# Kernel tuning notes

Hardware: AMD Instinct MI355X
Metric: run time of the kernel (lower is better)

The kernel has to match this reference:

```python
import jax, jax.numpy as jnp
import numpy as np

N = 100000
E = 1600000
IN_C = 128
HID_C = 32
HEADS = 4
OUT_C = 64
NUM_CLASSES = 2
NUM_GRAPHS = 64
NEG_SLOPE = 0.2  # PyG GATConv default leaky_relu slope


def _segment_softmax(logits, seg, num_segments):
    # logits: [E, H], seg: [E] destination node ids
    m = jax.ops.segment_max(logits, seg, num_segments=num_segments)
    m = jnp.where(jnp.isfinite(m), m, 0.0)
    e = jnp.exp(logits - m[seg])
    s = jax.ops.segment_sum(e, seg, num_segments=num_segments)
    return e / (s[seg] + 1e-16)


def _gat_conv(x, src, dst, W, att_src, att_dst, bias, heads, ch, concat):
    n = x.shape[0]
    h = (x @ W).reshape(n, heads, ch)                 # [N, H, C]
    a_src = jnp.sum(h * att_src, axis=-1)             # [N, H]
    a_dst = jnp.sum(h * att_dst, axis=-1)             # [N, H]
    alpha = jax.nn.leaky_relu(a_src[src] + a_dst[dst], NEG_SLOPE)  # [E, H]
    alpha = _segment_softmax(alpha, dst, n)
    msg = h[src] * alpha[:, :, None]                  # [E, H, C]
    out = jax.ops.segment_sum(msg, dst, num_segments=n)  # [N, H, C]
    out = out.reshape(n, heads * ch) if concat else out.mean(axis=1)
    return out + bias


def setup_inputs() -> dict:
    key = jax.random.key(0)
    ks = jax.random.split(key, 12)
    x = jax.random.normal(ks[0], (N, IN_C), dtype=jnp.float32)
    edge_index = jax.random.randint(ks[1], (2, E), 0, N, dtype=jnp.int32)
    batch = jnp.sort(jax.random.randint(ks[2], (N,), 0, NUM_GRAPHS, dtype=jnp.int32))
    s1 = 1.0 / np.sqrt(IN_C)
    W1 = jax.random.uniform(ks[3], (IN_C, HEADS * HID_C), minval=-s1, maxval=s1, dtype=jnp.float32)
    att_src1 = jax.random.normal(ks[4], (HEADS, HID_C), dtype=jnp.float32) * 0.1
    att_dst1 = jax.random.normal(ks[5], (HEADS, HID_C), dtype=jnp.float32) * 0.1
    b1 = jnp.zeros((HEADS * HID_C,), dtype=jnp.float32)
    s2 = 1.0 / np.sqrt(HEADS * HID_C)
    W2 = jax.random.uniform(ks[6], (HEADS * HID_C, OUT_C), minval=-s2, maxval=s2, dtype=jnp.float32)
    att_src2 = jax.random.normal(ks[7], (1, OUT_C), dtype=jnp.float32) * 0.1
    att_dst2 = jax.random.normal(ks[8], (1, OUT_C), dtype=jnp.float32) * 0.1
    b2 = jnp.zeros((OUT_C,), dtype=jnp.float32)
    sc = 1.0 / np.sqrt(OUT_C)
    Wc = jax.random.uniform(ks[9], (OUT_C, NUM_CLASSES), minval=-sc, maxval=sc, dtype=jnp.float32)
    bc = jnp.zeros((NUM_CLASSES,), dtype=jnp.float32)
    return {"x": x, "edge_index": edge_index, "batch": batch,
            "W1": W1, "att_src1": att_src1, "att_dst1": att_dst1, "b1": b1,
            "W2": W2, "att_src2": att_src2, "att_dst2": att_dst2, "b2": b2,
            "Wc": Wc, "bc": bc}


def reference(x, edge_index, batch, W1, att_src1, att_dst1, b1,
              W2, att_src2, att_dst2, b2, Wc, bc):
    # PyG GATConv adds self-loops by default
    loops = jnp.arange(N, dtype=edge_index.dtype)
    src = jnp.concatenate([edge_index[0], loops])
    dst = jnp.concatenate([edge_index[1], loops])
    # eval mode: dropout is identity
    h = _gat_conv(x, src, dst, W1, att_src1, att_dst1, b1, HEADS, HID_C, True)
    h = jax.nn.elu(h)
    h = _gat_conv(h, src, dst, W2, att_src2, att_dst2, b2, 1, OUT_C, False)
    h = jax.nn.elu(h)
    # global mean pool over graphs
    sums = jax.ops.segment_sum(h, batch, num_segments=NUM_GRAPHS)
    cnts = jax.ops.segment_sum(jnp.ones((N, 1), h.dtype), batch, num_segments=NUM_GRAPHS)
    pooled = sums / jnp.maximum(cnts, 1.0)
    return pooled @ Wc + bc
```

## Files before the change

### kernel.cpp

```cpp
#include <hip/hip_runtime.h>
#include <math.h>


typedef __attribute__((ext_vector_type(8))) short bf16x8;
typedef __attribute__((ext_vector_type(4))) float f32x4;

__device__ __forceinline__ unsigned f2bf_rne(float x){
  unsigned u = __float_as_uint(x);
  return (u + 0x7fffu + ((u >> 16) & 1u)) >> 16;
}
__device__ __forceinline__ unsigned pk_bf2(float a, float b){
  return f2bf_rne(a) | (f2bf_rne(b) << 16);
}
__device__ __forceinline__ void unpack8(uint4 q, float* f){
  f[0] = __uint_as_float(q.x << 16);
  f[1] = __uint_as_float(q.x & 0xffff0000u);
  f[2] = __uint_as_float(q.y << 16);
  f[3] = __uint_as_float(q.y & 0xffff0000u);
  f[4] = __uint_as_float(q.z << 16);
  f[5] = __uint_as_float(q.z & 0xffff0000u);
  f[6] = __uint_as_float(q.w << 16);
  f[7] = __uint_as_float(q.w & 0xffff0000u);
}


#define CHUNKE 8192

__global__ __launch_bounds__(256) void k_bucketcount(
    const int* __restrict__ dst, int* __restrict__ bcnt, int e, int NB)
{
  __shared__ int hcnt[512];
  const int tid = threadIdx.x;
  for (int b = tid; b < 512; b += 256) hcnt[b] = 0;
  __syncthreads();
  const int lo = blockIdx.x * CHUNKE;
  const int hi = min(lo + CHUNKE, e);
  for (int i = lo + tid; i < hi; i += 256)
    atomicAdd(&hcnt[dst[i] >> 8], 1);
  __syncthreads();
  for (int b = tid; b < NB; b += 256)
    if (hcnt[b]) atomicAdd(&bcnt[b], hcnt[b]);
}

__global__ __launch_bounds__(512) void k_bucketscan(
    const int* __restrict__ bcnt, int* __restrict__ bbase,
    int* __restrict__ cur, int* __restrict__ off, int e, int n, int NB)
{
  __shared__ int sh[512];
  const int t = threadIdx.x;
  int v = (t < NB) ? bcnt[t] : 0;
  sh[t] = v;
  __syncthreads();
  for (int o = 1; o < 512; o <<= 1){
    int x = (t >= o) ? sh[t - o] : 0;
    __syncthreads();
    sh[t] += x;
    __syncthreads();
  }
  if (t < NB){
    int excl = sh[t] - v;
    bbase[t] = excl;
    cur[t]   = excl;
  }
  if (t == 0) off[n] = e;
}

__global__ __launch_bounds__(256) void k_partition(
    const int* __restrict__ src, const int* __restrict__ dst,
    int* __restrict__ cur, unsigned* __restrict__ packed, int e, int NB)
{
  __shared__ unsigned       recs[CHUNKE];
  __shared__ unsigned short bkt[CHUNKE];
  __shared__ int hcnt[512];
  __shared__ int hoff[512];
  __shared__ int hbase[512];

  const int tid = threadIdx.x;
  const int lo  = blockIdx.x * CHUNKE;
  const int hi  = min(lo + CHUNKE, e);
  const int cnt = hi - lo;

  hcnt[tid] = 0; hcnt[tid + 256] = 0;
  __syncthreads();
  for (int i = lo + tid; i < hi; i += 256)
    atomicAdd(&hcnt[dst[i] >> 8], 1);
  __syncthreads();

  hoff[tid] = hcnt[tid]; hoff[tid + 256] = hcnt[tid + 256];
  __syncthreads();
  for (int o = 1; o < 512; o <<= 1){
    int x0 = (tid >= o)       ? hoff[tid - o]       : 0;
    int x1 = (tid + 256 >= o) ? hoff[tid + 256 - o] : 0;
    __syncthreads();
    hoff[tid] += x0; hoff[tid + 256] += x1;
    __syncthreads();
  }

  int c0 = hcnt[tid], c1 = hcnt[tid + 256];
  int e0 = hoff[tid] - c0, e1 = hoff[tid + 256] - c1;
  hbase[tid]       = c0 ? atomicAdd(&cur[tid], c0)       : 0;
  hbase[tid + 256] = c1 ? atomicAdd(&cur[tid + 256], c1) : 0;
  __syncthreads();
  hoff[tid] = e0; hoff[tid + 256] = e1;
  hcnt[tid] = 0;  hcnt[tid + 256] = 0;
  __syncthreads();

  for (int i = lo + tid; i < hi; i += 256){
    int d = dst[i];
    int b = d >> 8;
    int p = hoff[b] + atomicAdd(&hcnt[b], 1);
    recs[p] = (unsigned)src[i] | ((unsigned)(d & 255) << 17);
    bkt[p]  = (unsigned short)b;
  }
  __syncthreads();

  for (int t = tid; t < cnt; t += 256){
    int b = bkt[t];
    packed[hbase[b] + t - hoff[b]] = recs[t];
  }
}

__global__ __launch_bounds__(256) void k_bucketbuild(
    const unsigned* __restrict__ packed, const int* __restrict__ bbase,
    const int* __restrict__ bcnt, int* __restrict__ off,
    int* __restrict__ csr, int n)
{
  __shared__ int lcnt[256];
  __shared__ int loff[256];
  const int b    = blockIdx.x;
  const int tid  = threadIdx.x;
  const int seg0 = bbase[b];
  const int scnt = bcnt[b];

  lcnt[tid] = 0;
  __syncthreads();
  for (int i = tid; i < scnt; i += 256)
    atomicAdd(&lcnt[packed[seg0 + i] >> 17], 1);
  __syncthreads();
  int v = lcnt[tid];
  loff[tid] = v;
  __syncthreads();
  for (int o = 1; o < 256; o <<= 1){
    int x = (tid >= o) ? loff[tid - o] : 0;
    __syncthreads();
    loff[tid] += x;
    __syncthreads();
  }
  int excl = loff[tid] - v;
  __syncthreads();
  loff[tid] = excl;
  lcnt[tid] = 0;
  int d = (b << 8) + tid;
  if (d < n) off[d] = seg0 + excl;
  __syncthreads();
  for (int i = tid; i < scnt; i += 256){
    unsigned rec = packed[seg0 + i];
    int doff = rec >> 17;
    int s    = rec & 0x1FFFF;
    int p    = atomicAdd(&lcnt[doff], 1);
    csr[seg0 + loff[doff] + p] = s;
  }
}


template<int OUTC, int HEADS, bool XBF16, typename XT>
__global__ __launch_bounds__(256) void k_gemm_mfma(
    const XT* __restrict__ X, const float* __restrict__ W,
    const float* __restrict__ att_s, const float* __restrict__ att_d,
    unsigned short* __restrict__ H, float* __restrict__ ASRC,
    float* __restrict__ ADST, int n)
{
  constexpr int K  = 128;
  constexpr int KC = 32;
  constexpr int CT = OUTC / 16;
  constexpr int RT = 16 / CT;
  constexpr int WROWS = RT * 16;
  constexpr int BROWS = WROWS * 4;

  __shared__ unsigned short Bs[OUTC][K + 8];
  __shared__ unsigned short As[BROWS][KC + 8];

  const int tid   = threadIdx.x;
  const int lane  = tid & 63;
  const int c15   = lane & 15;
  const int quad  = lane >> 4;
  const int warow = (tid >> 6) * WROWS;
  const int row0  = blockIdx.x * BROWS;

  f32x4 acc[CT][RT];
  #pragma unroll
  for (int ct = 0; ct < CT; ++ct)
    #pragma unroll
    for (int t = 0; t < RT; ++t)
      #pragma unroll
      for (int r = 0; r < 4; ++r) acc[ct][t][r] = 0.f;

  for (int idx = tid; idx < K * OUTC / 4; idx += 256){
    int k  = idx / (OUTC / 4);
    int c4 = (idx % (OUTC / 4)) * 4;
    float4 v = *(const float4*)&W[(size_t)k * OUTC + c4];
    Bs[c4 + 0][k] = (unsigned short)f2bf_rne(v.x);
    Bs[c4 + 1][k] = (unsigned short)f2bf_rne(v.y);
    Bs[c4 + 2][k] = (unsigned short)f2bf_rne(v.z);
    Bs[c4 + 3][k] = (unsigned short)f2bf_rne(v.w);
  }

  for (int kc = 0; kc < K; kc += KC){
    if (XBF16){
      for (int idx = tid; idx < BROWS * (KC / 8); idx += 256){
        int rr = idx / (KC / 8);
        int q  = idx % (KC / 8);
        int row = row0 + rr;
        uint4 v = make_uint4(0, 0, 0, 0);
        if (row < n) v = *(const uint4*)((const unsigned short*)X + (size_t)row * K + kc + q * 8);
        *(uint4*)&As[rr][q * 8] = v;
      }
    } else {
      for (int idx = tid; idx < BROWS * (KC / 4); idx += 256){
        int rr = idx / (KC / 4);
        int q  = idx % (KC / 4);
        int row = row0 + rr;
        float4 v = make_float4(0.f, 0.f, 0.f, 0.f);
        if (row < n) v = *(const float4*)((const float*)X + (size_t)row * K + kc + q * 4);
        *(uint2*)&As[rr][q * 4] = make_uint2(pk_bf2(v.x, v.y), pk_bf2(v.z, v.w));
      }
    }
    __syncthreads();

    bf16x8 af[RT];
    #pragma unroll
    for (int t = 0; t < RT; ++t)
      af[t] = *(const bf16x8*)&As[warow + t * 16 + c15][8 * quad];
    #pragma unroll
    for (int ct = 0; ct < CT; ++ct){
      bf16x8 bfr = *(const bf16x8*)&Bs[ct * 16 + c15][kc + 8 * quad];
      #pragma unroll
      for (int t = 0; t < RT; ++t)
        acc[ct][t] = __builtin_amdgcn_mfma_f32_16x16x32_bf16(af[t], bfr, acc[ct][t], 0, 0, 0);
    }
    __syncthreads();
  }

  float ats[CT], atd[CT];
  #pragma unroll
  for (int ct = 0; ct < CT; ++ct){
    ats[ct] = att_s[ct * 16 + c15];
    atd[ct] = att_d[ct * 16 + c15];
  }
  #pragma unroll
  for (int t = 0; t < RT; ++t){
    #pragma unroll
    for (int r = 0; r < 4; ++r){
      int row = row0 + warow + t * 16 + quad * 4 + r;
      float hs[HEADS], hd[HEADS];
      #pragma unroll
      for (int h = 0; h < HEADS; ++h){ hs[h] = 0.f; hd[h] = 0.f; }
      #pragma unroll
      for (int ct = 0; ct < CT; ++ct){
        float v = acc[ct][t][r];
        constexpr int CPH = OUTC / HEADS;
        int h = (ct * 16) / CPH;
        hs[h] = fmaf(v, ats[ct], hs[h]);
        hd[h] = fmaf(v, atd[ct], hd[h]);
      }
      #pragma unroll
      for (int h = 0; h < HEADS; ++h){
        #pragma unroll
        for (int s = 1; s < 16; s <<= 1){
          hs[h] += __shfl_xor(hs[h], s);
          hd[h] += __shfl_xor(hd[h], s);
        }
      }
      if (row < n){
        #pragma unroll
        for (int ct = 0; ct < CT; ++ct)
          H[(size_t)row * OUTC + ct * 16 + c15] = (unsigned short)f2bf_rne(acc[ct][t][r]);
        if (c15 == 0){
          #pragma unroll
          for (int h = 0; h < HEADS; ++h){
            ASRC[(size_t)row * HEADS + h] = hs[h];
            ADST[(size_t)row * HEADS + h] = hd[h];
          }
        }
      }
    }
  }
}


template<int CH, int HEADS, bool OUTBF16>
__global__ __launch_bounds__(256) void k_aggregate(
    const unsigned short* __restrict__ Hmsg, const float* __restrict__ ASRC,
    const float* __restrict__ ADST, const int* __restrict__ off,
    const int* __restrict__ csr, const float* __restrict__ bias,
    void* __restrict__ OUT, int n)
{
  constexpr int CL  = CH / 8;
  constexpr int DPB = 256 / CL;
  constexpr int CPH = CH / HEADS;
  constexpr int RQ  = CH / 8;

  const int tid = threadIdx.x;
  const int ld  = tid / CL;
  const int cl  = tid % CL;
  const int c0  = cl * 8;
  const int h   = c0 / CPH;
  const int d   = blockIdx.x * DPB + ld;
  if (d >= n) return;

  const uint4* Hv = (const uint4*)Hmsg;
  const float adst = ADST[d * HEADS + h];

  float acc[8];
  float wsum;
  {
    float t = ASRC[d * HEADS + h] + adst;
    float w = __expf(fmaxf(t, 0.2f * t));
    float f[8];
    unpack8(Hv[d * RQ + cl], f);
    #pragma unroll
    for (int j = 0; j < 8; ++j) acc[j] = w * f[j];
    wsum = w;
  }

  const int s0   = off[d];
  const int cnt  = off[d + 1] - s0;
  const int full = cnt & ~7;

  for (int p = 0; p < full; p += 8){
    int idx[8];
    #pragma unroll
    for (int j = 0; j < 8; ++j) idx[j] = csr[s0 + p + j];
    float av[8];
    #pragma unroll
    for (int j = 0; j < 8; ++j) av[j] = ASRC[idx[j] * HEADS + h];
    uint4 hq[8];
    #pragma unroll
    for (int j = 0; j < 8; ++j) hq[j] = Hv[idx[j] * RQ + cl];
    #pragma unroll
    for (int j = 0; j < 8; ++j){
      float t = av[j] + adst;
      float w = __expf(fmaxf(t, 0.2f * t));
      float f[8];
      unpack8(hq[j], f);
      #pragma unroll
      for (int q = 0; q < 8; ++q) acc[q] = fmaf(w, f[q], acc[q]);
      wsum += w;
    }
  }

  const int rem = cnt - full;
  if (rem){
    int  idx[8];
    bool ok[8];
    #pragma unroll
    for (int j = 0; j < 8; ++j){
      int q = csr[s0 + full + j];
      ok[j]  = j < rem;
      idx[j] = ok[j] ? q : 0;
    }
    float av[8];
    #pragma unroll
    for (int j = 0; j < 8; ++j) av[j] = ASRC[idx[j] * HEADS + h];
    uint4 hq[8];
    #pragma unroll
    for (int j = 0; j < 8; ++j) hq[j] = Hv[idx[j] * RQ + cl];
    #pragma unroll
    for (int j = 0; j < 8; ++j){
      float t = av[j] + adst;
      float w = __expf(fmaxf(t, 0.2f * t));
      w = ok[j] ? w : 0.f;
      float f[8];
      unpack8(hq[j], f);
      #pragma unroll
      for (int q = 0; q < 8; ++q) acc[q] = fmaf(w, f[q], acc[q]);
      wsum += w;
    }
  }

  const float inv = 1.f / (wsum + 1e-16f);
  float o[8];
  #pragma unroll
  for (int j = 0; j < 8; ++j){
    float v = acc[j] * inv + bias[c0 + j];
    o[j] = v > 0.f ? v : expm1f(v);
  }
  if (OUTBF16){
    uint4 q;
    q.x = pk_bf2(o[0], o[1]); q.y = pk_bf2(o[2], o[3]);
    q.z = pk_bf2(o[4], o[5]); q.w = pk_bf2(o[6], o[7]);
    *(uint4*)((unsigned short*)OUT + (size_t)d * CH + c0) = q;
  } else {
    float* Of = (float*)OUT;
    *(float4*)&Of[(size_t)d * CH + c0 + 0] = make_float4(o[0], o[1], o[2], o[3]);
    *(float4*)&Of[(size_t)d * CH + c0 + 4] = make_float4(o[4], o[5], o[6], o[7]);
  }
}


__global__ __launch_bounds__(256) void k_pool_partial(
    const float* __restrict__ H, const int* __restrict__ batch,
    float* __restrict__ sums, int n)
{
  constexpr int CHUNK = 256;
  const int c    = threadIdx.x & 63;
  const int slot = threadIdx.x >> 6;
  const int start = blockIdx.x * CHUNK;
  const int end   = min(start + CHUNK, n);

  float acc = 0.f;
  int cur = -1;
  for (int nn = start + slot; nn < end; nn += 4){
    int g = batch[nn];
    if (g != cur){
      if (cur >= 0) atomicAdd(&sums[cur * 64 + c], acc);
      acc = 0.f; cur = g;
    }
    acc += H[(size_t)nn * 64 + c];
  }
  if (cur >= 0) atomicAdd(&sums[cur * 64 + c], acc);
}

__global__ __launch_bounds__(128) void k_classify(
    const float* __restrict__ sums, const int* __restrict__ batch,
    const float* __restrict__ Wc, const float* __restrict__ bc,
    float* __restrict__ out, int n)
{
  int t = threadIdx.x;
  if (t >= 128) return;
  int g = t >> 1, cls = t & 1;
  int lo = 0, hi = n;
  while (lo < hi){ int m = (lo + hi) >> 1; if (batch[m] < g) lo = m + 1; else hi = m; }
  int s = lo;
  lo = s; hi = n;
  while (lo < hi){ int m = (lo + hi) >> 1; if (batch[m] < g + 1) lo = m + 1; else hi = m; }
  int cnt = lo - s;
  float inv = 1.f / (float)(cnt > 1 ? cnt : 1);
  float dot = 0.f;
  #pragma unroll
  for (int c = 0; c < 64; ++c) dot = fmaf(sums[g * 64 + c], Wc[c * 2 + cls], dot);
  out[g * 2 + cls] = dot * inv + bc[cls];
}


extern "C" void kernel_launch(void* const* d_in, const int* in_sizes, int n_in,
                              void* d_out, int out_size, void* d_ws, size_t ws_size,
                              hipStream_t stream)
{
  const float* x    = (const float*)d_in[0];
  const int*   edge = (const int*)  d_in[1];
  const int*   batch= (const int*)  d_in[2];
  const float* W1   = (const float*)d_in[3];
  const float* as1w = (const float*)d_in[4];
  const float* ad1w = (const float*)d_in[5];
  const float* b1   = (const float*)d_in[6];
  const float* W2   = (const float*)d_in[7];
  const float* as2w = (const float*)d_in[8];
  const float* ad2w = (const float*)d_in[9];
  const float* b2   = (const float*)d_in[10];
  const float* Wc   = (const float*)d_in[11];
  const float* bc   = (const float*)d_in[12];

  const int n = in_sizes[2];
  const int e = in_sizes[1] / 2;
  const int* esrc = edge;
  const int* edst = edge + e;
  const int NB = (n + 255) >> 8;

  unsigned short* h1  = (unsigned short*)d_ws;
  unsigned short* h1a = h1 + (size_t)n * 128;
  float* as1 = (float*)(h1a + (size_t)n * 128);
  float* ad1 = as1 + (size_t)n * 4;
  float* as2 = ad1 + (size_t)n * 4;
  float* ad2 = as2 + (size_t)n;
  float* sums = ad2 + (size_t)n;
  int*  bcnt  = (int*)(sums + 64 * 64);
  int*  cur   = bcnt + 512;
  int*  bbase = cur + 512;
  int*  off   = bbase + 512;
  unsigned* packed = (unsigned*)(off + n + 1);
  int*  csr   = (int*)(packed + e);

  const int eb = (e + CHUNKE - 1) / CHUNKE;

  hipMemsetAsync(sums, 0, (64 * 64 + 512) * 4, stream);
  k_bucketcount<<<eb, 256, 0, stream>>>(edst, bcnt, e, NB);
  k_bucketscan <<<1, 512, 0, stream>>>(bcnt, bbase, cur, off, e, n, NB);
  k_partition  <<<eb, 256, 0, stream>>>(esrc, edst, cur, packed, e, NB);
  k_bucketbuild<<<NB, 256, 0, stream>>>(packed, bbase, bcnt, off, csr, n);

  k_gemm_mfma<128, 4, false><<<(n + 127) / 128, 256, 0, stream>>>(
      x, W1, as1w, ad1w, h1, as1, ad1, n);
  k_aggregate<128, 4, true><<<(n + 15) / 16, 256, 0, stream>>>(
      h1, as1, ad1, off, csr, b1, (void*)h1a, n);

  unsigned short* h2 = h1;
  float* h2a = (float*)h1a;
  k_gemm_mfma<64, 1, true><<<(n + 255) / 256, 256, 0, stream>>>(
      h1a, W2, as2w, ad2w, h2, as2, ad2, n);
  k_aggregate<64, 1, false><<<(n + 31) / 32, 256, 0, stream>>>(
      h2, as2, ad2, off, csr, b2, (void*)h2a, n);

  k_pool_partial<<<(n + 255) / 256, 256, 0, stream>>>(h2a, batch, sums, n);
  k_classify<<<1, 128, 0, stream>>>(sums, batch, Wc, bc, (float*)d_out, n);
}
```

Measured before the change: 376.3 us.

## Fold attention vectors into GEMM as extra MFMA tile; multi-dst aggregate

Precomputes W·att_src and W·att_dst per head, stored as hi/lo bf16 split rows, inside an otherwise idle second block of the scan kernel. The GEMM then gets the attention logits from one extra 16-column MFMA tile instead of a per-row shuffle reduction over heads. The aggregate kernels also process four destination nodes per thread group with bias hoisted, cutting block count. This trades an extra MFMA tile and bf16-split precision for fewer shuffles, and adds serial per-thread work that may reduce latency hiding in the aggregation.

```diff
diff --git a/kernel.cpp b/kernel.cpp
--- a/kernel.cpp
+++ b/kernel.cpp
@@ -44,10 +44,56 @@
 
 __global__ __launch_bounds__(512) void k_bucketscan(
     const int* __restrict__ bcnt, int* __restrict__ bbase,
-    int* __restrict__ cur, int* __restrict__ off, int e, int n, int NB)
-{
+    int* __restrict__ cur, int* __restrict__ off, int e, int n, int NB,
+    const float* __restrict__ W1, const float* __restrict__ as1w,
+    const float* __restrict__ ad1w,
+    const float* __restrict__ W2, const float* __restrict__ as2w,
+    const float* __restrict__ ad2w,
+    unsigned short* __restrict__ wa1, unsigned short* __restrict__ wa2)
+{
+  const int t = threadIdx.x;
+
+  if (blockIdx.x == 1){
+    for (int i = t; i < 2048; i += 512) wa2[i] = 0;
+    __syncthreads();
+    {
+      int k = t >> 2, j = t & 3;
+      float ds = 0.f, dd = 0.f;
+      for (int cc = 0; cc < 32; ++cc){
+        float wv = W1[k * 128 + j * 32 + cc];
+        ds = fmaf(wv, as1w[j * 32 + cc], ds);
+        dd = fmaf(wv, ad1w[j * 32 + cc], dd);
+      }
+      unsigned hs_ = f2bf_rne(ds); float hsf = __uint_as_float(hs_ << 16);
+      unsigned ls_ = f2bf_rne(ds - hsf);
+      unsigned hd_ = f2bf_rne(dd); float hdf = __uint_as_float(hd_ << 16);
+      unsigned ld_ = f2bf_rne(dd - hdf);
+      wa1[(j     ) * 128 + k] = (unsigned short)hs_;
+      wa1[(j + 4 ) * 128 + k] = (unsigned short)ls_;
+      wa1[(j + 8 ) * 128 + k] = (unsigned short)hd_;
+      wa1[(j + 12) * 128 + k] = (unsigned short)ld_;
+    }
+    if (t < 128){
+      int k = t;
+      float ds = 0.f, dd = 0.f;
+      for (int cc = 0; cc < 64; ++cc){
+        float wv = W2[k * 64 + cc];
+        ds = fmaf(wv, as2w[cc], ds);
+        dd = fmaf(wv, ad2w[cc], dd);
+      }
+      unsigned hs_ = f2bf_rne(ds); float hsf = __uint_as_float(hs_ << 16);
+      unsigned ls_ = f2bf_rne(ds - hsf);
+      unsigned hd_ = f2bf_rne(dd); float hdf = __uint_as_float(hd_ << 16);
+      unsigned ld_ = f2bf_rne(dd - hdf);
+      wa2[ 0 * 128 + k] = (unsigned short)hs_;
+      wa2[ 4 * 128 + k] = (unsigned short)ls_;
+      wa2[ 8 * 128 + k] = (unsigned short)hd_;
+      wa2[12 * 128 + k] = (unsigned short)ld_;
+    }
+    return;
+  }
+
   __shared__ int sh[512];
-  const int t = threadIdx.x;
   int v = (t < NB) ? bcnt[t] : 0;
   sh[t] = v;
   __syncthreads();
@@ -166,18 +212,19 @@
 template<int OUTC, int HEADS, bool XBF16, typename XT>
 __global__ __launch_bounds__(256) void k_gemm_mfma(
     const XT* __restrict__ X, const float* __restrict__ W,
-    const float* __restrict__ att_s, const float* __restrict__ att_d,
+    const unsigned short* __restrict__ WATT,
     unsigned short* __restrict__ H, float* __restrict__ ASRC,
     float* __restrict__ ADST, int n)
 {
   constexpr int K  = 128;
   constexpr int KC = 32;
   constexpr int CT = OUTC / 16;
+  constexpr int CTX = CT + 1;
   constexpr int RT = 16 / CT;
   constexpr int WROWS = RT * 16;
   constexpr int BROWS = WROWS * 4;
 
-  __shared__ unsigned short Bs[OUTC][K + 8];
+  __shared__ unsigned short Bs[OUTC + 16][K + 8];
   __shared__ unsigned short As[BROWS][KC + 8];
 
   const int tid   = threadIdx.x;
@@ -187,9 +234,9 @@
   const int warow = (tid >> 6) * WROWS;
   const int row0  = blockIdx.x * BROWS;
 
-  f32x4 acc[CT][RT];
+  f32x4 acc[CTX][RT];
   #pragma unroll
-  for (int ct = 0; ct < CT; ++ct)
+  for (int ct = 0; ct < CTX; ++ct)
     #pragma unroll
     for (int t = 0; t < RT; ++t)
       #pragma unroll
@@ -203,6 +250,11 @@
     Bs[c4 + 1][k] = (unsigned short)f2bf_rne(v.y);
     Bs[c4 + 2][k] = (unsigned short)f2bf_rne(v.z);
     Bs[c4 + 3][k] = (unsigned short)f2bf_rne(v.w);
+  }
+  for (int idx = tid; idx < 16 * (K / 8); idx += 256){
+    int rr = idx >> 4;
+    int q  = idx & 15;
+    *(uint4*)&Bs[OUTC + rr][q * 8] = *(const uint4*)&WATT[rr * K + q * 8];
   }
 
   for (int kc = 0; kc < K; kc += KC){
@@ -232,7 +284,7 @@
     for (int t = 0; t < RT; ++t)
       af[t] = *(const bf16x8*)&As[warow + t * 16 + c15][8 * quad];
     #pragma unroll
-    for (int ct = 0; ct < CT; ++ct){
+    for (int ct = 0; ct < CTX; ++ct){
       bf16x8 bfr = *(const bf16x8*)&Bs[ct * 16 + c15][kc + 8 * quad];
       #pragma unroll
       for (int t = 0; t < RT; ++t)
@@ -241,54 +293,26 @@
     __syncthreads();
   }
 
-  float ats[CT], atd[CT];
-  #pragma unroll
-  for (int ct = 0; ct < CT; ++ct){
-    ats[ct] = att_s[ct * 16 + c15];
-    atd[ct] = att_d[ct * 16 + c15];
-  }
   #pragma unroll
   for (int t = 0; t < RT; ++t){
     #pragma unroll
     for (int r = 0; r < 4; ++r){
       int row = row0 + warow + t * 16 + quad * 4 + r;
-      float hs[HEADS], hd[HEADS];
-      #pragma unroll
-      for (int h = 0; h < HEADS; ++h){ hs[h] = 0.f; hd[h] = 0.f; }
-      #pragma unroll
-      for (int ct = 0; ct < CT; ++ct){
-        float v = acc[ct][t][r];
-        constexpr int CPH = OUTC / HEADS;
-        int h = (ct * 16) / CPH;
-        hs[h] = fmaf(v, ats[ct], hs[h]);
-        hd[h] = fmaf(v, atd[ct], hd[h]);
-      }
-      #pragma unroll
-      for (int h = 0; h < HEADS; ++h){
-        #pragma unroll
-        for (int s = 1; s < 16; s <<= 1){
-          hs[h] += __shfl_xor(hs[h], s);
-          hd[h] += __shfl_xor(hd[h], s);
-        }
-      }
+      float av = acc[CT][t][r];
+      av += __shfl_xor(av, 4);
       if (row < n){
         #pragma unroll
         for (int ct = 0; ct < CT; ++ct)
           H[(size_t)row * OUTC + ct * 16 + c15] = (unsigned short)f2bf_rne(acc[ct][t][r]);
-        if (c15 == 0){
-          #pragma unroll
-          for (int h = 0; h < HEADS; ++h){
-            ASRC[(size_t)row * HEADS + h] = hs[h];
-            ADST[(size_t)row * HEADS + h] = hd[h];
-          }
-        }
-      }
-    }
-  }
-}
-
-
-template<int CH, int HEADS, bool OUTBF16>
+        if (c15 < HEADS)                      ASRC[row * HEADS + c15] = av;
+        else if (c15 >= 8 && c15 < 8 + HEADS) ADST[row * HEADS + c15 - 8] = av;
+      }
+    }
+  }
+}
+
+
+template<int CH, int HEADS, bool OUTBF16, int DSTS>
 __global__ __launch_bounds__(256) void k_aggregate(
     const unsigned short* __restrict__ Hmsg, const float* __restrict__ ASRC,
     const float* __restrict__ ADST, const int* __restrict__ off,
@@ -296,104 +320,112 @@
     void* __restrict__ OUT, int n)
 {
   constexpr int CL  = CH / 8;
-  constexpr int DPB = 256 / CL;
+  constexpr int GPB = 256 / CL;
   constexpr int CPH = CH / HEADS;
   constexpr int RQ  = CH / 8;
 
   const int tid = threadIdx.x;
-  const int ld  = tid / CL;
   const int cl  = tid % CL;
   const int c0  = cl * 8;
   const int h   = c0 / CPH;
-  const int d   = blockIdx.x * DPB + ld;
-  if (d >= n) return;
-
+  const int g   = blockIdx.x * GPB + tid / CL;
   const uint4* Hv = (const uint4*)Hmsg;
-  const float adst = ADST[d * HEADS + h];
-
-  float acc[8];
-  float wsum;
-  {
-    float t = ASRC[d * HEADS + h] + adst;
-    float w = __expf(fmaxf(t, 0.2f * t));
-    float f[8];
-    unpack8(Hv[d * RQ + cl], f);
-    #pragma unroll
-    for (int j = 0; j < 8; ++j) acc[j] = w * f[j];
-    wsum = w;
-  }
-
-  const int s0   = off[d];
-  const int cnt  = off[d + 1] - s0;
-  const int full = cnt & ~7;
-
-  for (int p = 0; p < full; p += 8){
-    int idx[8];
-    #pragma unroll
-    for (int j = 0; j < 8; ++j) idx[j] = csr[s0 + p + j];
-    float av[8];
-    #pragma unroll
-    for (int j = 0; j < 8; ++j) av[j] = ASRC[idx[j] * HEADS + h];
-    uint4 hq[8];
-    #pragma unroll
-    for (int j = 0; j < 8; ++j) hq[j] = Hv[idx[j] * RQ + cl];
+
+  float bv[8];
+  #pragma unroll
+  for (int j = 0; j < 8; ++j) bv[j] = bias[c0 + j];
+
+  #pragma unroll 1
+  for (int it = 0; it < DSTS; ++it){
+    const int d = g * DSTS + it;
+    if (d >= n) break;
+
+    const float adst = ADST[d * HEADS + h];
+
+    float acc[8];
+    float wsum;
+    {
+      float t = ASRC[d * HEADS + h] + adst;
+      float w = __expf(fmaxf(t, 0.2f * t));
+      float f[8];
+      unpack8(Hv[d * RQ + cl], f);
+      #pragma unroll
+      for (int j = 0; j < 8; ++j) acc[j] = w * f[j];
+      wsum = w;
+    }
+
+    const int s0   = off[d];
+    const int cnt  = off[d + 1] - s0;
+    const int full = cnt & ~7;
+
+    for (int p = 0; p < full; p += 8){
+      int idx[8];
+      #pragma unroll
+      for (int j = 0; j < 8; ++j) idx[j] = csr[s0 + p + j];
+      float av[8];
+      #pragma unroll
+      for (int j = 0; j < 8; ++j) av[j] = ASRC[idx[j] * HEADS + h];
+      uint4 hq[8];
+      #pragma unroll
+      for (int j = 0; j < 8; ++j) hq[j] = Hv[idx[j] * RQ + cl];
+      #pragma unroll
+      for (int j = 0; j < 8; ++j){
+        float t = av[j] + adst;
+        float w = __expf(fmaxf(t, 0.2f * t));
+        float f[8];
+        unpack8(hq[j], f);
+        #pragma unroll
+        for (int q = 0; q < 8; ++q) acc[q] = fmaf(w, f[q], acc[q]);
+        wsum += w;
+      }
+    }
+
+    const int rem = cnt - full;
+    if (rem){
+      int  idx[8];
+      bool ok[8];
+      #pragma unroll
+      for (int j = 0; j < 8; ++j){
+        int q = csr[s0 + full + j];
+        ok[j]  = j < rem;
+        idx[j] = ok[j] ? q : 0;
+      }
+      float av[8];
+      #pragma unroll
+      for (int j = 0; j < 8; ++j) av[j] = ASRC[idx[j] * HEADS + h];
+      uint4 hq[8];
+      #pragma unroll
+      for (int j = 0; j < 8; ++j) hq[j] = Hv[idx[j] * RQ + cl];
+      #pragma unroll
+      for (int j = 0; j < 8; ++j){
+        float t = av[j] + adst;
+        float w = __expf(fmaxf(t, 0.2f * t));
+        w = ok[j] ? w : 0.f;
+        float f[8];
+        unpack8(hq[j], f);
+        #pragma unroll
+        for (int q = 0; q < 8; ++q) acc[q] = fmaf(w, f[q], acc[q]);
+        wsum += w;
+      }
+    }
+
+    const float inv = 1.f / (wsum + 1e-16f);
+    float o[8];
     #pragma unroll
     for (int j = 0; j < 8; ++j){
-      float t = av[j] + adst;
-      float w = __expf(fmaxf(t, 0.2f * t));
-      float f[8];
-      unpack8(hq[j], f);
-      #pragma unroll
-      for (int q = 0; q < 8; ++q) acc[q] = fmaf(w, f[q], acc[q]);
-      wsum += w;
-    }
-  }
-
-  const int rem = cnt - full;
-  if (rem){
-    int  idx[8];
-    bool ok[8];
-    #pragma unroll
-    for (int j = 0; j < 8; ++j){
-      int q = csr[s0 + full + j];
-      ok[j]  = j < rem;
-      idx[j] = ok[j] ? q : 0;
-    }
-    float av[8];
-    #pragma unroll
-    for (int j = 0; j < 8; ++j) av[j] = ASRC[idx[j] * HEADS + h];
-    uint4 hq[8];
-    #pragma unroll
-    for (int j = 0; j < 8; ++j) hq[j] = Hv[idx[j] * RQ + cl];
-    #pragma unroll
-    for (int j = 0; j < 8; ++j){
-      float t = av[j] + adst;
-      float w = __expf(fmaxf(t, 0.2f * t));
-      w = ok[j] ? w : 0.f;
-      float f[8];
-      unpack8(hq[j], f);
-      #pragma unroll
-      for (int q = 0; q < 8; ++q) acc[q] = fmaf(w, f[q], acc[q]);
-      wsum += w;
-    }
-  }
-
-  const float inv = 1.f / (wsum + 1e-16f);
-  float o[8];
-  #pragma unroll
-  for (int j = 0; j < 8; ++j){
-    float v = acc[j] * inv + bias[c0 + j];
-    o[j] = v > 0.f ? v : expm1f(v);
-  }
-  if (OUTBF16){
-    uint4 q;
-    q.x = pk_bf2(o[0], o[1]); q.y = pk_bf2(o[2], o[3]);
-    q.z = pk_bf2(o[4], o[5]); q.w = pk_bf2(o[6], o[7]);
-    *(uint4*)((unsigned short*)OUT + (size_t)d * CH + c0) = q;
-  } else {
-    float* Of = (float*)OUT;
-    *(float4*)&Of[(size_t)d * CH + c0 + 0] = make_float4(o[0], o[1], o[2], o[3]);
-    *(float4*)&Of[(size_t)d * CH + c0 + 4] = make_float4(o[4], o[5], o[6], o[7]);
+      float v = acc[j] * inv + bv[j];
+      o[j] = v > 0.f ? v : expm1f(v);
+    }
+    if (OUTBF16){
+      uint4 q;
+      q.x = pk_bf2(o[0], o[1]); q.y = pk_bf2(o[2], o[3]);
+      q.z = pk_bf2(o[4], o[5]); q.w = pk_bf2(o[6], o[7]);
+      *(uint4*)((unsigned short*)OUT + (size_t)d * CH + c0) = q;
+    } else {
+      float* Of = (float*)OUT;
+      *(float4*)&Of[(size_t)d * CH + c0 + 0] = make_float4(o[0], o[1], o[2], o[3]);
+      *(float4*)&Of[(size_t)d * CH + c0 + 4] = make_float4(o[4], o[5], o[6], o[7]);
+    }
   }
 }
 
@@ -474,7 +506,9 @@
   float* as2 = ad1 + (size_t)n * 4;
   float* ad2 = as2 + (size_t)n;
   float* sums = ad2 + (size_t)n;
-  int*  bcnt  = (int*)(sums + 64 * 64);
+  unsigned short* wa1 = (unsigned short*)(sums + 64 * 64);
+  unsigned short* wa2 = wa1 + 2048;
+  int*  bcnt  = (int*)(wa2 + 2048);
   int*  cur   = bcnt + 512;
   int*  bbase = cur + 512;
   int*  off   = bbase + 512;
@@ -483,22 +517,23 @@
 
   const int eb = (e + CHUNKE - 1) / CHUNKE;
 
-  hipMemsetAsync(sums, 0, (64 * 64 + 512) * 4, stream);
+  hipMemsetAsync(sums, 0, 64 * 64 * 4 + 2 * 4096 + 512 * 4, stream);
   k_bucketcount<<<eb, 256, 0, stream>>>(edst, bcnt, e, NB);
-  k_bucketscan <<<1, 512, 0, stream>>>(bcnt, bbase, cur, off, e, n, NB);
+  k_bucketscan <<<2, 512, 0, stream>>>(bcnt, bbase, cur, off, e, n, NB,
+                                       W1, as1w, ad1w, W2, as2w, ad2w, wa1, wa2);
   k_partition  <<<eb, 256, 0, stream>>>(esrc, edst, cur, packed, e, NB);
   k_bucketbuild<<<NB, 256, 0, stream>>>(packed, bbase, bcnt, off, csr, n);
 
   k_gemm_mfma<128, 4, false><<<(n + 127) / 128, 256, 0, stream>>>(
-      x, W1, as1w, ad1w, h1, as1, ad1, n);
-  k_aggregate<128, 4, true><<<(n + 15) / 16, 256, 0, stream>>>(
+      x, W1, wa1, h1, as1, ad1, n);
+  k_aggregate<128, 4, true, 4><<<(n + 63) / 64, 256, 0, stream>>>(
       h1, as1, ad1, off, csr, b1, (void*)h1a, n);
 
   unsigned short* h2 = h1;
   float* h2a = (float*)h1a;
   k_gemm_mfma<64, 1, true><<<(n + 255) / 256, 256, 0, stream>>>(
-      h1a, W2, as2w, ad2w, h2, as2, ad2, n);
-  k_aggregate<64, 1, false><<<(n + 31) / 32, 256, 0, stream>>>(
+      h1a, W2, wa2, h2, as2, ad2, n);
+  k_aggregate<64, 1, false, 4><<<(n + 127) / 128, 256, 0, stream>>>(
       h2, as2, ad2, off, csr, b2, (void*)h2a, n);
 
   k_pool_partial<<<(n + 255) / 256, 256, 0, stream>>>(h2a, batch, sums, n);
```

Result: no change. 375.9 us (-0.1%).
